# Kernel optimization log

Measured on AMD Instinct MI355X. Metric: run time of the kernel, lower is better.

The kernel has to match this reference:

```python
import jax, jax.numpy as jnp
import numpy as np

B = 64            # batch_size
A = 128           # max_ligand_atoms
D = 128           # embed_dim
TOTAL = 262144    # total virtual nodes across batch (~4096 per sample)
MAXV = 4608       # static pad width for per-batch virtual nodes (>= max bincount)


def setup_inputs() -> dict:
    key = jax.random.key(0)
    k1, k2, k3, k4, k5 = jax.random.split(key, 5)
    virtual_embeddings = jax.random.normal(k1, (TOTAL, D), dtype=jnp.float32)
    virtual_coords = jax.random.normal(k2, (TOTAL, 3), dtype=jnp.float32)
    target_mask = jax.random.randint(k3, (B, A), 0, 2).astype(bool)
    batch_idx = jnp.sort(jax.random.randint(k4, (TOTAL,), 0, B, dtype=jnp.int64))
    W_w = jax.random.normal(k5, (1, D), dtype=jnp.float32) * 0.05
    b_w = jnp.zeros((1,), dtype=jnp.float32)
    return {"virtual_embeddings": virtual_embeddings,
            "virtual_coords": virtual_coords,
            "target_mask": target_mask,
            "batch_idx": batch_idx,
            "W_w": W_w,
            "b_w": b_w}


def reference(virtual_embeddings, virtual_coords, target_mask, batch_idx, W_w, b_w):
    bi = batch_idx.astype(jnp.int32)
    scale = 1.0
    # logits: Linear(embed_dim -> num_heads), take head 0  -> [TOTAL]
    logits = scale * (virtual_embeddings @ W_w[0] + b_w[0])
    # segmented (per-batch) stable softmax over virtual nodes
    seg_max = jax.ops.segment_max(logits, bi, num_segments=B)          # [B]
    seg_max = jnp.where(jnp.isfinite(seg_max), seg_max, 0.0)           # empty segments
    z = jnp.exp(logits - seg_max[bi])                                  # [TOTAL]
    seg_sum = jax.ops.segment_sum(z, bi, num_segments=B)               # [B]
    denom = jnp.where(seg_sum > 0, seg_sum, 1.0)
    w = z / denom[bi]                                                  # [TOTAL]
    # per-batch softmax-weighted coordinate sum -> [B, 3]
    coord_b = jax.ops.segment_sum(w[:, None] * virtual_coords, bi, num_segments=B)
    maskf = target_mask.astype(virtual_embeddings.dtype)               # [B, A]
    # broadcast the identical per-batch coord to every masked atom
    predicted_coords = coord_b[:, None, :] * maskf[:, :, None]         # [B, A, 3]
    # padded per-batch weights: position of each node within its segment (sorted batch_idx)
    counts = jax.ops.segment_sum(jnp.ones_like(w), bi, num_segments=B)
    starts = jnp.concatenate([jnp.zeros((1,), counts.dtype),
                              jnp.cumsum(counts)[:-1]])
    pos = (jnp.arange(TOTAL) - starts[bi].astype(jnp.int32)).astype(jnp.int32)
    pos = jnp.minimum(pos, MAXV - 1)
    padded = jnp.zeros((B, MAXV), virtual_embeddings.dtype).at[bi, pos].set(w)
    attention_weights_all = padded[:, None, :] * maskf[:, :, None]     # [B, A, MAXV]
    return predicted_coords, attention_weights_all
```

## Files before the change

### kernel.cpp

```cpp
#include <hip/hip_runtime.h>
#include <math.h>

#define TOTAL 262144
#define BATCH 64
#define ATOMS 128
#define DIM   128
#define MAXV  4608

typedef float vf4 __attribute__((ext_vector_type(4)));

#define WS_Z      0
#define WS_ACC    (TOTAL)
#define WS_STARTS (TOTAL + BATCH * 4)
#define WS_FLAGS  (WS_STARTS + BATCH + 1)

__device__ __forceinline__ int load_bi(const void* bi_raw, int idx, int is64) {
    return is64 ? (int)(((const long long*)bi_raw)[idx])
                : ((const int*)bi_raw)[idx];
}

__global__ __launch_bounds__(256) void k_fused(const vf4* __restrict__ emb4,
                                               const float* __restrict__ coords,
                                               const void* __restrict__ bi_raw,
                                               const void* __restrict__ mask_raw,
                                               const vf4* __restrict__ W4,
                                               const float* __restrict__ b_w,
                                               float* __restrict__ z_out,
                                               float* __restrict__ acc,
                                               int* __restrict__ starts,
                                               int* __restrict__ flags) {
    const int tid   = threadIdx.x;
    const int l16   = tid & 15;
    const int group = tid >> 4;
    const int CHUNK = 128;
    const int chunk0 = blockIdx.x * CHUNK;

    __shared__ float bins[BATCH * 4];
    for (int i = tid; i < BATCH * 4; i += 256) bins[i] = 0.f;

    const int is64 = (((const int*)bi_raw)[TOTAL - 1] == 0) ? 1 : 0;

    if (blockIdx.x == 0) {
        int isByte = 0;
        for (int i = tid; i < (BATCH * ATOMS) / 4; i += 256) {
            unsigned w = ((const unsigned*)mask_raw)[i];
            if (w > 1u) isByte = 1;
        }
        if (isByte) atomicOr(flags, 1);
    }

    if (tid < CHUNK) {
        int node = chunk0 + tid;
        int b = load_bi(bi_raw, node, is64);
        int bp = (node == 0) ? -1 : load_bi(bi_raw, node - 1, is64);
        if (b != bp) starts[b] = node;
        if (node == TOTAL - 1) starts[BATCH] = TOTAL;
    }
    __syncthreads();

    const vf4 w0 = W4[l16];
    const vf4 w1 = W4[16 + l16];
    const float bias = b_w[0];

    float accV = 0.f;
    int curb = -1;
    const int role = l16;

    #pragma unroll 4
    for (int it = 0; it < CHUNK / 16; ++it) {
        int node = chunk0 + it * 16 + group;
        const vf4* row = emb4 + node * (DIM / 4);
        vf4 v0 = __builtin_nontemporal_load(&row[l16]);
        vf4 v1 = __builtin_nontemporal_load(&row[16 + l16]);
        float d = v0.x * w0.x + v0.y * w0.y + v0.z * w0.z + v0.w * w0.w
                + v1.x * w1.x + v1.y * w1.y + v1.z * w1.z + v1.w * w1.w;
        #pragma unroll
        for (int m = 8; m >= 1; m >>= 1) d += __shfl_xor(d, m, 16);
        float z = __expf(d + bias);
        if (role < 4) {
            int b = load_bi(bi_raw, node, is64);
            float val = (role == 0) ? z : z * coords[3 * node + (role - 1)];
            if (role == 0) z_out[node] = z;
            if (b != curb) {
                if (curb >= 0) atomicAdd(&bins[curb * 4 + role], accV);
                curb = b;
                accV = 0.f;
            }
            accV += val;
        }
    }
    if (role < 4 && curb >= 0)
        atomicAdd(&bins[curb * 4 + role], accV);
    __syncthreads();
    for (int i = tid; i < BATCH * 4; i += 256) {
        float v = bins[i];
        if (v != 0.f) atomicAdd(&acc[i], v);
    }
}

__device__ __forceinline__ void emit_row4(vf4* __restrict__ dst,
                                          const float* __restrict__ z,
                                          int s, int n, float inv, int v4) {
    int v = v4 * 4;
    vf4 o;
    o.x = (v + 0 < n) ? z[s + v + 0] * inv : 0.f;
    o.y = (v + 1 < n) ? z[s + v + 1] * inv : 0.f;
    o.z = (v + 2 < n) ? z[s + v + 2] * inv : 0.f;
    o.w = (v + 3 < n) ? z[s + v + 3] * inv : 0.f;
    if (n > MAXV && v4 == MAXV / 4 - 1) o.w = z[s + n - 1] * inv;
    __builtin_nontemporal_store(o, &dst[v4]);
}

__global__ __launch_bounds__(256) void k_bcast(const float* __restrict__ z,
                                               const float* __restrict__ acc,
                                               const int* __restrict__ starts,
                                               const int* __restrict__ flags,
                                               const void* __restrict__ mask_raw,
                                               float* __restrict__ out0,
                                               vf4* __restrict__ out1_4) {
    const int bid = blockIdx.x;
    const int tid = threadIdx.x;
    const int b = bid >> 7;
    const int a = bid & (ATOMS - 1);

    __shared__ float s_inv;
    __shared__ int s_m, s_s, s_n, s_byte;
    if (tid == 0) {
        int isByte = flags[0];
        s_byte = isByte;
        s_m = isByte ? (int)(((const unsigned char*)mask_raw)[bid])
                     : ((((const int*)mask_raw)[bid]) != 0);
        float S = acc[b * 4];
        s_inv = 1.f / ((S > 0.f) ? S : 1.f);
        s_s = starts[b];
        s_n = starts[b + 1] - starts[b];
    }
    __syncthreads();

    vf4* dst = out1_4 + (size_t)bid * (MAXV / 4);
    if (!s_m) {
        vf4 zz = (vf4)(0.f);
        #pragma unroll
        for (int k = 0; k < 4; ++k)
            __builtin_nontemporal_store(zz, &dst[tid + k * 256]);
        if (tid < 128)
            __builtin_nontemporal_store(zz, &dst[tid + 1024]);
    } else {
        const int s = s_s, n = s_n;
        const float inv = s_inv;
        #pragma unroll
        for (int k = 0; k < 4; ++k)
            emit_row4(dst, z, s, n, inv, tid + k * 256);
        if (tid < 128)
            emit_row4(dst, z, s, n, inv, tid + 1024);
    }

    if (a == 0) {
        const float inv = s_inv;
        const int isByte = s_byte;
        float c0 = acc[b * 4 + 1] * inv;
        float c1 = acc[b * 4 + 2] * inv;
        float c2 = acc[b * 4 + 3] * inv;
        for (int j = tid; j < ATOMS * 3; j += 256) {
            int at = j / 3, c = j - 3 * at;
            int mv = isByte ? (int)(((const unsigned char*)mask_raw)[b * ATOMS + at])
                            : ((((const int*)mask_raw)[b * ATOMS + at]) != 0);
            __builtin_nontemporal_store(
                mv ? (c == 0 ? c0 : (c == 1 ? c1 : c2)) : 0.f,
                &out0[b * ATOMS * 3 + j]);
        }
    }
}

extern "C" void kernel_launch(void* const* d_in, const int* in_sizes, int n_in,
                              void* d_out, int out_size, void* d_ws, size_t ws_size,
                              hipStream_t stream) {
    const float* emb    = (const float*)d_in[0];
    const float* coords = (const float*)d_in[1];
    const void*  mask   = d_in[2];
    const void*  bi     = d_in[3];
    const float* W      = (const float*)d_in[4];
    const float* bw     = (const float*)d_in[5];

    float* wsf    = (float*)d_ws;
    float* z      = wsf + WS_Z;
    float* acc    = wsf + WS_ACC;
    int*   starts = (int*)(wsf + WS_STARTS);
    int*   flags  = (int*)(wsf + WS_FLAGS);

    float* out0 = (float*)d_out;
    float* out1 = out0 + BATCH * ATOMS * 3;

    (void)hipMemsetAsync(acc, 0, (BATCH * 4 + BATCH + 1 + 1) * sizeof(float), stream);

    hipLaunchKernelGGL(k_fused, dim3(TOTAL / 128), dim3(256), 0, stream,
                       (const vf4*)emb, coords, bi, mask,
                       (const vf4*)W, bw, z, acc, starts, flags);
    hipLaunchKernelGGL(k_bcast, dim3(BATCH * ATOMS), dim3(256), 0, stream,
                       z, acc, starts, flags, mask, out0, (vf4*)out1);
}
```

Before: 260.3 us.

## Move segment reductions into broadcast kernel and drop atomics and memset

The first kernel now only computes exp(logits) and segment starts. It no longer uses shared-memory bins or global atomic accumulation, so the memset launch goes away. Each broadcast block recomputes its segment's sum of z with a block reduction, and the a==0 blocks also compute the coordinate-weighted sums. This removes atomics and one launch, but every masked block now rereads about 4K z values, which is redundant work served mostly from cache.

```diff
diff --git a/kernel.cpp b/kernel.cpp
--- a/kernel.cpp
+++ b/kernel.cpp
@@ -10,8 +10,7 @@
 typedef float vf4 __attribute__((ext_vector_type(4)));
 
 #define WS_Z      0
-#define WS_ACC    (TOTAL)
-#define WS_STARTS (TOTAL + BATCH * 4)
+#define WS_STARTS (TOTAL)
 #define WS_FLAGS  (WS_STARTS + BATCH + 1)
 
 __device__ __forceinline__ int load_bi(const void* bi_raw, int idx, int is64) {
@@ -19,55 +18,49 @@
                 : ((const int*)bi_raw)[idx];
 }
 
-__global__ __launch_bounds__(256) void k_fused(const vf4* __restrict__ emb4,
-                                               const float* __restrict__ coords,
-                                               const void* __restrict__ bi_raw,
-                                               const void* __restrict__ mask_raw,
-                                               const vf4* __restrict__ W4,
-                                               const float* __restrict__ b_w,
-                                               float* __restrict__ z_out,
-                                               float* __restrict__ acc,
-                                               int* __restrict__ starts,
-                                               int* __restrict__ flags) {
+__global__ __launch_bounds__(256) void k_logits(const vf4* __restrict__ emb4,
+                                                const void* __restrict__ bi_raw,
+                                                const void* __restrict__ mask_raw,
+                                                const vf4* __restrict__ W4,
+                                                const float* __restrict__ b_w,
+                                                float* __restrict__ z_out,
+                                                int* __restrict__ starts,
+                                                int* __restrict__ flags) {
     const int tid   = threadIdx.x;
     const int l16   = tid & 15;
     const int group = tid >> 4;
-    const int CHUNK = 128;
-    const int chunk0 = blockIdx.x * CHUNK;
-
-    __shared__ float bins[BATCH * 4];
-    for (int i = tid; i < BATCH * 4; i += 256) bins[i] = 0.f;
+    const int chunk0 = blockIdx.x * 128;
 
     const int is64 = (((const int*)bi_raw)[TOTAL - 1] == 0) ? 1 : 0;
 
     if (blockIdx.x == 0) {
+        __shared__ int sb;
+        if (tid == 0) sb = 0;
+        __syncthreads();
         int isByte = 0;
         for (int i = tid; i < (BATCH * ATOMS) / 4; i += 256) {
             unsigned w = ((const unsigned*)mask_raw)[i];
             if (w > 1u) isByte = 1;
         }
-        if (isByte) atomicOr(flags, 1);
+        if (isByte) atomicOr(&sb, 1);
+        __syncthreads();
+        if (tid == 0) flags[0] = sb;
     }
 
-    if (tid < CHUNK) {
+    if (tid < 128) {
         int node = chunk0 + tid;
         int b = load_bi(bi_raw, node, is64);
         int bp = (node == 0) ? -1 : load_bi(bi_raw, node - 1, is64);
         if (b != bp) starts[b] = node;
         if (node == TOTAL - 1) starts[BATCH] = TOTAL;
     }
-    __syncthreads();
 
     const vf4 w0 = W4[l16];
     const vf4 w1 = W4[16 + l16];
     const float bias = b_w[0];
 
-    float accV = 0.f;
-    int curb = -1;
-    const int role = l16;
-
-    #pragma unroll 4
-    for (int it = 0; it < CHUNK / 16; ++it) {
+    #pragma unroll
+    for (int it = 0; it < 8; ++it) {
         int node = chunk0 + it * 16 + group;
         const vf4* row = emb4 + node * (DIM / 4);
         vf4 v0 = __builtin_nontemporal_load(&row[l16]);
@@ -76,26 +69,17 @@
                 + v1.x * w1.x + v1.y * w1.y + v1.z * w1.z + v1.w * w1.w;
         #pragma unroll
         for (int m = 8; m >= 1; m >>= 1) d += __shfl_xor(d, m, 16);
-        float z = __expf(d + bias);
-        if (role < 4) {
-            int b = load_bi(bi_raw, node, is64);
-            float val = (role == 0) ? z : z * coords[3 * node + (role - 1)];
-            if (role == 0) z_out[node] = z;
-            if (b != curb) {
-                if (curb >= 0) atomicAdd(&bins[curb * 4 + role], accV);
-                curb = b;
-                accV = 0.f;
-            }
-            accV += val;
-        }
+        if (l16 == 0) z_out[node] = __expf(d + bias);
     }
-    if (role < 4 && curb >= 0)
-        atomicAdd(&bins[curb * 4 + role], accV);
+}
+
+__device__ __forceinline__ float block_sum256(float v, float* red, int tid) {
+    #pragma unroll
+    for (int m = 32; m >= 1; m >>= 1) v += __shfl_xor(v, m);
     __syncthreads();
-    for (int i = tid; i < BATCH * 4; i += 256) {
-        float v = bins[i];
-        if (v != 0.f) atomicAdd(&acc[i], v);
-    }
+    if ((tid & 63) == 0) red[tid >> 6] = v;
+    __syncthreads();
+    return (red[0] + red[1]) + (red[2] + red[3]);
 }
 
 __device__ __forceinline__ void emit_row4(vf4* __restrict__ dst,
@@ -112,7 +96,7 @@
 }
 
 __global__ __launch_bounds__(256) void k_bcast(const float* __restrict__ z,
-                                               const float* __restrict__ acc,
+                                               const float* __restrict__ coords,
                                                const int* __restrict__ starts,
                                                const int* __restrict__ flags,
                                                const void* __restrict__ mask_raw,
@@ -123,22 +107,30 @@
     const int b = bid >> 7;
     const int a = bid & (ATOMS - 1);
 
-    __shared__ float s_inv;
-    __shared__ int s_m, s_s, s_n, s_byte;
+    __shared__ float red[4];
+    __shared__ int sh[4];
     if (tid == 0) {
         int isByte = flags[0];
-        s_byte = isByte;
-        s_m = isByte ? (int)(((const unsigned char*)mask_raw)[bid])
-                     : ((((const int*)mask_raw)[bid]) != 0);
-        float S = acc[b * 4];
-        s_inv = 1.f / ((S > 0.f) ? S : 1.f);
-        s_s = starts[b];
-        s_n = starts[b + 1] - starts[b];
+        sh[3] = isByte;
+        sh[2] = isByte ? (int)(((const unsigned char*)mask_raw)[bid])
+                       : ((((const int*)mask_raw)[bid]) != 0);
+        int s0 = starts[b];
+        sh[0] = s0;
+        sh[1] = starts[b + 1] - s0;
     }
     __syncthreads();
+    const int s = sh[0], n = sh[1], m = sh[2], isByte = sh[3];
+
+    float inv = 1.f;
+    if (m || a == 0) {
+        float acc = 0.f;
+        for (int i = tid; i < n; i += 256) acc += z[s + i];
+        float S = block_sum256(acc, red, tid);
+        inv = 1.f / ((S > 0.f) ? S : 1.f);
+    }
 
     vf4* dst = out1_4 + (size_t)bid * (MAXV / 4);
-    if (!s_m) {
+    if (!m) {
         vf4 zz = (vf4)(0.f);
         #pragma unroll
         for (int k = 0; k < 4; ++k)
@@ -146,8 +138,6 @@
         if (tid < 128)
             __builtin_nontemporal_store(zz, &dst[tid + 1024]);
     } else {
-        const int s = s_s, n = s_n;
-        const float inv = s_inv;
         #pragma unroll
         for (int k = 0; k < 4; ++k)
             emit_row4(dst, z, s, n, inv, tid + k * 256);
@@ -156,11 +146,17 @@
     }
 
     if (a == 0) {
-        const float inv = s_inv;
-        const int isByte = s_byte;
-        float c0 = acc[b * 4 + 1] * inv;
-        float c1 = acc[b * 4 + 2] * inv;
-        float c2 = acc[b * 4 + 3] * inv;
+        float a0 = 0.f, a1 = 0.f, a2 = 0.f;
+        for (int i = tid; i < n; i += 256) {
+            int node = s + i;
+            float zz = z[node];
+            a0 += zz * coords[3 * node + 0];
+            a1 += zz * coords[3 * node + 1];
+            a2 += zz * coords[3 * node + 2];
+        }
+        float c0 = block_sum256(a0, red, tid) * inv;
+        float c1 = block_sum256(a1, red, tid) * inv;
+        float c2 = block_sum256(a2, red, tid) * inv;
         for (int j = tid; j < ATOMS * 3; j += 256) {
             int at = j / 3, c = j - 3 * at;
             int mv = isByte ? (int)(((const unsigned char*)mask_raw)[b * ATOMS + at])
@@ -184,18 +180,15 @@
 
     float* wsf    = (float*)d_ws;
     float* z      = wsf + WS_Z;
-    float* acc    = wsf + WS_ACC;
     int*   starts = (int*)(wsf + WS_STARTS);
     int*   flags  = (int*)(wsf + WS_FLAGS);
 
     float* out0 = (float*)d_out;
     float* out1 = out0 + BATCH * ATOMS * 3;
 
-    (void)hipMemsetAsync(acc, 0, (BATCH * 4 + BATCH + 1 + 1) * sizeof(float), stream);
-
-    hipLaunchKernelGGL(k_fused, dim3(TOTAL / 128), dim3(256), 0, stream,
-                       (const vf4*)emb, coords, bi, mask,
-                       (const vf4*)W, bw, z, acc, starts, flags);
+    hipLaunchKernelGGL(k_logits, dim3(TOTAL / 128), dim3(256), 0, stream,
+                       (const vf4*)emb, bi, mask,
+                       (const vf4*)W, bw, z, starts, flags);
     hipLaunchKernelGGL(k_bcast, dim3(BATCH * ATOMS), dim3(256), 0, stream,
-                       z, acc, starts, flags, mask, out0, (vf4*)out1);
+                       z, coords, starts, flags, mask, out0, (vf4*)out1);
 }
```

New measurement: 299.3 us. 1.15x slower.
